# Performance work log

Measured on AMD Instinct MI355X. Metric: run time of the kernel, lower is better.

Reference implementation:

```python
import jax, jax.numpy as jnp
import numpy as np

NC = 80          # num classes (len(yolov8.names))
CONF = 0.25      # ultralytics conf_thres default
IOU_T = 0.45     # ultralytics iou_thres default
MAX_DET = 300    # module default max_det
K = 1024         # pre-NMS candidate cap (static stand-in for max_nms)
MAX_WH = 7680.0  # ultralytics class-offset for multi-class NMS


def setup_inputs() -> dict:
    key = jax.random.key(0)
    k1, k2, k3 = jax.random.split(key, 3)
    B, A = 32, 8400
    # YOLOv8 head layout: rows 0:4 = xywh (pixels), rows 4: = sigmoid class scores
    xy = jax.random.uniform(k1, (B, 2, A), dtype=jnp.float32) * 640.0
    wh = jax.random.uniform(k2, (B, 2, A), dtype=jnp.float32) * 160.0 + 8.0
    scores = jax.random.uniform(k3, (B, NC, A), dtype=jnp.float32) ** 3  # mostly below conf_thres
    preds = jnp.concatenate([xy, wh, scores], axis=1)  # [B, 4+NC, A]
    return {"preds": preds}


def _box_iou(b):
    # b: [K, 4] xyxy -> [K, K] pairwise IoU
    area = (b[:, 2] - b[:, 0]) * (b[:, 3] - b[:, 1])
    lt = jnp.maximum(b[:, None, :2], b[None, :, :2])
    rb = jnp.minimum(b[:, None, 2:], b[None, :, 2:])
    wh = jnp.clip(rb - lt, 0.0)
    inter = wh[..., 0] * wh[..., 1]
    return inter / (area[:, None] + area[None, :] - inter + 1e-7)


def _nms_single(pred):
    # pred: [4+NC, A]
    boxes_xywh = pred[:4].T           # [A, 4]
    cls_scores = pred[4:].T           # [A, NC]
    conf = cls_scores.max(-1)         # best-class confidence per anchor
    cls = jnp.argmax(cls_scores, -1)
    score = jnp.where(conf > CONF, conf, 0.0)
    top, idx = jax.lax.top_k(score, K)            # K candidates by confidence
    xywh = boxes_xywh[idx]
    half = xywh[:, 2:] * 0.5
    boxes = jnp.concatenate([xywh[:, :2] - half, xywh[:, :2] + half], -1)  # xyxy
    cls_k = cls[idx]
    valid = top > CONF
    # multi-class NMS via per-class coordinate offset (ultralytics trick)
    iou = _box_iou(boxes + (cls_k.astype(boxes.dtype) * MAX_WH)[:, None])
    ar = jnp.arange(K)

    def body(i, st):
        supp, keep = st
        ki = valid[i] & ~supp[i]
        keep = keep.at[i].set(ki)
        supp = supp | (ki & (iou[i] > IOU_T) & (ar > i))
        return supp, keep

    _, keep = jax.lax.fori_loop(0, K, body,
                                (jnp.zeros(K, bool), jnp.zeros(K, bool)))
    fscore = jnp.where(keep, top, 0.0)
    sc, order = jax.lax.top_k(fscore, MAX_DET)
    det = jnp.concatenate(
        [boxes[order], top[order][:, None], cls_k[order].astype(boxes.dtype)[:, None]], -1)
    # pad invalid rows with value NC in every column (matches F.pad(value=len(names)))
    return jnp.where((sc > CONF)[:, None], det, jnp.float32(NC))


def reference(preds):
    # [B, MAX_DET, 6] -> (x1, y1, x2, y2, conf, cls), padded rows filled with NC
    return jax.vmap(_nms_single)(preds)
```

## Files before the change

### kernel.cpp

```cpp
#include <hip/hip_runtime.h>
#include <stdint.h>

typedef unsigned long long u64;
typedef unsigned int u32;

#define NC 80
#define CONF_T 0.25f
#define IOU_THR 0.45f
#define MAX_DET 300
#define KBIG 1024
#define A_ANCH 8400
#define NROWS 84
#define MAX_WH 7680.0f
#define HBINS 256
#define BIN_BASE 0x3e80u

__device__ __forceinline__ void hadd(u32* h, u32 bin, bool m, int lane) {
    u64 act = __ballot(m);
    if (act == 0) return;
    int fl = __ffsll((unsigned long long)act) - 1;
    u32 fb = __shfl(bin, fl);
    u64 same = __ballot(m && (bin == fb));
    if (lane == fl) atomicAdd(&h[fb], (u32)__popcll(same));
    if (m && (bin != fb)) atomicAdd(&h[bin], 1u);
}

__global__ __launch_bounds__(512) void yolo_conf_kernel(const float* __restrict__ preds,
                                                        u64* __restrict__ keys,
                                                        u32* __restrict__ hist) {
    int b = blockIdx.x / 9;
    int slab = blockIdx.x % 9;
    if (slab == 0 && threadIdx.x < HBINS) hist[(size_t)b * HBINS + threadIdx.x] = 0;
    int g = slab * 512 + threadIdx.x;
    if (g >= A_ANCH / 2) return;
    int a0 = g * 2;
    const float* base = preds + ((size_t)b * NROWS + 4) * A_ANCH + a0;
    float2 best = *(const float2*)base;
    int bc0 = 0, bc1 = 0;
#pragma unroll 8
    for (int c = 1; c < NC; ++c) {
        float2 v = *(const float2*)(base + (size_t)c * A_ANCH);
        if (v.x > best.x) { best.x = v.x; bc0 = c; }
        if (v.y > best.y) { best.y = v.y; bc1 = c; }
    }
    float s0 = (best.x > CONF_T) ? best.x : 0.0f;
    float s1 = (best.y > CONF_T) ? best.y : 0.0f;
    ulonglong2 kk;
    kk.x = ((u64)__float_as_uint(s0) << 32) | ((u64)(16383 - a0) << 7) | (u64)bc0;
    kk.y = ((u64)__float_as_uint(s1) << 32) | ((u64)(16383 - (a0 + 1)) << 7) | (u64)bc1;
    *(ulonglong2*)(keys + (size_t)b * A_ANCH + a0) = kk;
}

__global__ __launch_bounds__(256) void yolo_prep_kernel(const float* __restrict__ preds,
                                                        const u64* __restrict__ keys,
                                                        float4* __restrict__ obox,
                                                        u32* __restrict__ hist) {
    __shared__ u32 lh[HBINS];
    const int lane = threadIdx.x & 63;
    int b = blockIdx.x / 33;
    int a = (blockIdx.x % 33) * 256 + threadIdx.x;
    lh[threadIdx.x] = 0;
    __syncthreads();
    u32 bits = 0, bin = 0;
    bool act = a < A_ANCH;
    if (act) {
        u64 key = keys[(size_t)b * A_ANCH + a];
        bits = (u32)(key >> 32);
        int cls = (int)(key & 127u);
        const float* pb = preds + (size_t)b * NROWS * A_ANCH + a;
        float x = pb[0];
        float y = pb[A_ANCH];
        float w = pb[2 * A_ANCH];
        float h = pb[3 * A_ANCH];
        float hw = __fmul_rn(w, 0.5f), hh = __fmul_rn(h, 0.5f);
        float x1 = __fsub_rn(x, hw), x2 = __fadd_rn(x, hw);
        float y1 = __fsub_rn(y, hh), y2 = __fadd_rn(y, hh);
        float off = __fmul_rn((float)cls, MAX_WH);
        float4 oB;
        oB.x = __fadd_rn(x1, off); oB.y = __fadd_rn(y1, off);
        oB.z = __fadd_rn(x2, off); oB.w = __fadd_rn(y2, off);
        obox[(size_t)b * A_ANCH + a] = oB;
        bin = (bits >> 16) - BIN_BASE;
        if (bin > 255u) bin = 255u;
    }
    hadd(lh, bin, act && (bits != 0u), lane);
    __syncthreads();
    u32 c = lh[threadIdx.x];
    if (c) atomicAdd(&hist[(size_t)b * HBINS + threadIdx.x], c);
}

__device__ __forceinline__ float iou_f(float ix1, float iy1, float ix2, float iy2, float iar,
                                       float jx1, float jy1, float jx2, float jy2, float jar) {
    float lx = fmaxf(ix1, jx1), ly = fmaxf(iy1, jy1);
    float rx = fminf(ix2, jx2), ry = fminf(iy2, jy2);
    float ww = fmaxf(__fsub_rn(rx, lx), 0.0f);
    float hh = fmaxf(__fsub_rn(ry, ly), 0.0f);
    float inter = __fmul_rn(ww, hh);
    float den = __fadd_rn(__fsub_rn(__fadd_rn(iar, jar), inter), 1e-7f);
    return __fdiv_rn(inter, den);
}

__device__ __forceinline__ u64 bstep(u64 v, u32 idx, u32 size, u32 stride) {
    u64 v2 = __shfl_xor((unsigned long long)v, (int)stride, 64);
    bool keep_big = (((idx & stride) == 0) == ((idx & size) == 0));
    return ((v > v2) == keep_big) ? v : v2;
}

__device__ __forceinline__ void radix_scan(u32* hist, int nb, int shift, u32* s_scal,
                                           u32* wsum, int tid, int lane, int wid) {
    int per = nb >> 9; if (per == 0) per = 1;
    int na = nb / per;
    u32 rem = s_scal[1];
    u32 Pk = s_scal[0];
    int hi = nb - 1 - per * tid;
    u32 s = 0;
    if (tid < na)
        for (int q = 0; q < per; ++q) s += hist[hi - q];
    u32 pre = s;
#pragma unroll
    for (int off = 1; off < 64; off <<= 1) {
        u32 o = __shfl_up(pre, off);
        if (lane >= off) pre += o;
    }
    if (lane == 63) wsum[wid] = pre;
    __syncthreads();
    u32 base = 0;
    for (int w = 0; w < wid; ++w) base += wsum[w];
    u32 run = base + pre - s;
    if (tid < na) {
        for (int q = 0; q < per; ++q) {
            int d = hi - q;
            u32 g = hist[d];
            if (run < rem && rem <= run + g) {
                s_scal[0] = Pk | ((u32)d << shift);
                s_scal[1] = rem - run;
            }
            run += g;
        }
    }
    __syncthreads();
}

__global__ __launch_bounds__(512) void yolo_selsort_kernel(const u64* __restrict__ keys,
                                                           const u32* __restrict__ hist,
                                                           u64* __restrict__ sortk,
                                                           u32* __restrict__ meta) {
    const int b = blockIdx.x;
    const int tid = threadIdx.x;
    const int lane = tid & 63;
    const int wid = tid >> 6;

    __shared__ u64 skey[KBIG];
    __shared__ u32 wsum[8];
    __shared__ u32 s_scal[4];
    __shared__ u32 s_cnt;

    const u64* kb = keys + (size_t)b * A_ANCH;
    const u32* hb = hist + (size_t)b * HBINS;

    u32 hg = (tid < HBINS) ? hb[HBINS - 1 - tid] : 0u;
    u32 vals[17];
#pragma unroll
    for (int it = 0; it < 17; ++it) {
        int a = tid + it * 512;
        vals[it] = (a < A_ANCH) ? (u32)(kb[a] >> 32) : 0u;
    }
    {
        u32 pre = hg;
#pragma unroll
        for (int off = 1; off < 64; off <<= 1) {
            u32 o = __shfl_up(pre, off);
            if (lane >= off) pre += o;
        }
        if (lane == 63) wsum[wid] = pre;
        __syncthreads();
        u32 base = 0;
        for (int w = 0; w < wid; ++w) base += wsum[w];
        pre += base;
        u32 run = pre - hg;
        if (tid < HBINS) {
            if (run < 512u && 512u <= pre) { s_scal[0] = (u32)(HBINS - 1 - tid); s_scal[2] = pre; }
            if (tid == HBINS - 1) {
                s_scal[3] = pre;
                if (pre < 512u) { s_scal[0] = 0; s_scal[2] = pre; }
            }
        }
        __syncthreads();
    }
    const u32 Pbin16 = BIN_BASE + s_scal[0];
    const u32 Cfast = s_scal[2];
    const u32 validN = s_scal[3];
    if (tid == 0) { meta[b * 2] = Cfast; meta[b * 2 + 1] = validN; }
    if (Cfast > (u32)KBIG) return;

    skey[tid] = 0; skey[tid + 512] = 0;
    if (tid == 0) s_cnt = 0;
    __syncthreads();
#pragma unroll
    for (int it = 0; it < 17; ++it) {
        int a = tid + it * 512;
        u32 v = vals[it];
        bool take = (a < A_ANCH) && (v != 0u) && ((v >> 16) >= Pbin16);
        u64 m = __ballot(take);
        if (m) {
            int fl = __ffsll((unsigned long long)m) - 1;
            u32 basep = 0;
            if (lane == fl) basep = atomicAdd(&s_cnt, (u32)__popcll(m));
            basep = __shfl(basep, fl);
            if (take) {
                u32 pos = basep + (u32)__popcll(m & ((1ull << lane) - 1ull));
                if (pos < (u32)KBIG) skey[pos] = kb[a];
            }
        }
    }
    __syncthreads();

    {
        u64 vA = skey[tid], vB = skey[tid + 512];
        const u32 iA = (u32)tid, iB = (u32)tid + 512;
#pragma unroll
        for (u32 size = 2; size <= 64; size <<= 1)
#pragma unroll
            for (u32 stride = size >> 1; stride >= 1; stride >>= 1) {
                vA = bstep(vA, iA, size, stride);
                vB = bstep(vB, iB, size, stride);
            }
        skey[tid] = vA; skey[tid + 512] = vB;
        __syncthreads();
        for (u32 size = 128; size <= 1024; size <<= 1) {
            for (u32 stride = size >> 1; stride >= 64; stride >>= 1) {
                u32 i1 = ((tid & ~(int)(stride - 1)) << 1) | (tid & (stride - 1));
                u32 i2 = i1 + stride;
                bool desc = ((i1 & size) == 0);
                u64 x = skey[i1], y = skey[i2];
                if ((x < y) == desc) { skey[i1] = y; skey[i2] = x; }
                __syncthreads();
            }
            vA = skey[tid]; vB = skey[tid + 512];
#pragma unroll
            for (u32 stride = 32; stride >= 1; stride >>= 1) {
                vA = bstep(vA, iA, size, stride);
                vB = bstep(vB, iB, size, stride);
            }
            skey[tid] = vA; skey[tid + 512] = vB;
            __syncthreads();
        }
    }
    u64* so = sortk + (size_t)b * KBIG;
    so[tid] = skey[tid];
    so[tid + 512] = skey[tid + 512];
}

__global__ __launch_bounds__(512) void yolo_mat_kernel(const u64* __restrict__ sortk,
                                                       const float4* __restrict__ obox,
                                                       u64* __restrict__ rows) {
    const int b = blockIdx.x >> 3;
    const int m = blockIdx.x & 7;
    const int tid = threadIdx.x;
    const int lane = tid & 63;
    const int wid = tid >> 6;
    __shared__ float bx1[512], by1[512], bx2[512], by2[512], bar[512];

    const u64* sk = sortk + (size_t)b * KBIG;
    {
        u64 key = sk[tid];
        int idx = 16383 - (int)((key >> 7) & 16383u);
        if (idx >= A_ANCH || idx < 0) idx = 0;
        float4 ob = obox[(size_t)b * A_ANCH + idx];
        bx1[tid] = ob.x; by1[tid] = ob.y; bx2[tid] = ob.z; by2[tid] = ob.w;
        bar[tid] = __fmul_rn(__fsub_rn(ob.z, ob.x), __fsub_rn(ob.w, ob.y));
    }
    __syncthreads();

#pragma unroll
    for (int rr = 0; rr < 8; ++rr) {
        int i = m * 64 + wid * 8 + rr;
        float ix1 = bx1[i], iy1 = by1[i], ix2 = bx2[i], iy2 = by2[i], iar = bar[i];
        u64* rowp = rows + ((size_t)b * 512 + i) * 8;
#pragma unroll
        for (int wd = 0; wd < 8; ++wd) {
            int j = wd * 64 + lane;
            float iou = iou_f(ix1, iy1, ix2, iy2, iar, bx1[j], by1[j], bx2[j], by2[j], bar[j]);
            u64 mbit = __ballot((j > i) && (iou > IOU_THR));
            if (lane == 0) rowp[wd] = mbit;
        }
    }
}

__global__ __launch_bounds__(512) void yolo_rec_kernel(const float* __restrict__ preds,
                                                       const u64* __restrict__ sortk,
                                                       const u64* __restrict__ rows,
                                                       const u32* __restrict__ meta,
                                                       u32* __restrict__ done,
                                                       float* __restrict__ out) {
    const int b = blockIdx.x;
    const int tid = threadIdx.x;
    const int lane = tid & 63;
    const int wid = tid >> 6;
    __shared__ u64 skl[512];
    __shared__ u64 supp[8];
    __shared__ u64 s_keep;
    __shared__ int keptlist[364];
    __shared__ u32 s_nkept;

    const u32 Cfast = meta[b * 2];
    const u32 validN = meta[b * 2 + 1];
    skl[tid] = sortk[(size_t)b * KBIG + tid];
    if (tid < 8) supp[tid] = 0;
    if (tid == 0) s_nkept = 0;
    __syncthreads();

    bool ok = (Cfast <= (u32)KBIG);
    if (ok) {
        const u64* rb = rows + (size_t)b * 512 * 8;
        for (int c = 0; c < 8; ++c) {
            if (wid == 0) {
                int i = c * 64 + lane;
                u64 key = skl[i];
                float sc = __uint_as_float((u32)(key >> 32));
                u64 ri = rb[(size_t)i * 8 + c];
                u64 validm = __ballot(sc > CONF_T) & ~supp[c];
                u32 rlo = (u32)ri, rhi = (u32)(ri >> 32);
                u64 sup = 0, keep = 0;
#pragma unroll
                for (int i2 = 0; i2 < 64; ++i2) {
                    u64 rr = (((u64)(u32)__builtin_amdgcn_readlane((int)rhi, i2)) << 32) |
                             (u64)(u32)__builtin_amdgcn_readlane((int)rlo, i2);
                    bool ki = (((validm & ~sup) >> i2) & 1ull) != 0;
                    if (ki) { keep |= (1ull << i2); sup |= rr; }
                }
                u32 basek = s_nkept;
                if ((keep >> lane) & 1ull) {
                    u32 slot = basek + (u32)__popcll(keep & ((1ull << lane) - 1ull));
                    keptlist[slot] = i;
                }
                if (lane == 0) { s_keep = keep; s_nkept = basek + (u32)__popcll(keep); }
            }
            __syncthreads();
            {
                u64 k = s_keep;
                u64 t = ((k >> lane) & 1ull) ? rb[(size_t)(c * 64 + lane) * 8 + wid] : 0ull;
#pragma unroll
                for (int off = 32; off >= 1; off >>= 1)
                    t |= (u64)__shfl_xor((unsigned long long)t, off, 64);
                if (lane == 0) supp[wid] |= t;
            }
            __syncthreads();
            if (s_nkept >= MAX_DET) break;
        }
    }
    u32 nk = ok ? s_nkept : 0;
    bool fin = ok && ((nk >= MAX_DET) || (validN <= 512u));
    if (tid == 0) done[b] = fin ? 1u : 0u;
    if (!fin) return;

    if (tid < MAX_DET) {
        float row[6];
        int t = (tid < (int)(nk < MAX_DET ? nk : MAX_DET)) ? keptlist[tid] : -1;
        if (t >= 0) {
            u64 key = skl[t];
            float score = __uint_as_float((u32)(key >> 32));
            int cls = (int)(key & 127u);
            int idx = 16383 - (int)((key >> 7) & 16383u);
            if (idx >= A_ANCH || idx < 0) idx = 0;
            const float* pb = preds + (size_t)b * NROWS * A_ANCH + idx;
            float x = pb[0], y = pb[A_ANCH], w = pb[2 * A_ANCH], h = pb[3 * A_ANCH];
            float hw = __fmul_rn(w, 0.5f), hh = __fmul_rn(h, 0.5f);
            row[0] = __fsub_rn(x, hw);
            row[1] = __fsub_rn(y, hh);
            row[2] = __fadd_rn(x, hw);
            row[3] = __fadd_rn(y, hh);
            row[4] = score;
            row[5] = (float)cls;
        } else {
            row[0] = row[1] = row[2] = row[3] = row[4] = row[5] = (float)NC;
        }
        float* o = out + ((size_t)b * MAX_DET + tid) * 6;
#pragma unroll
        for (int q = 0; q < 6; ++q) o[q] = row[q];
    }
}

union U2 {
    u32 hist[4096];
    struct { u32 eqw[264]; u32 wpre[264]; } tie;
};

__global__ __launch_bounds__(512) void yolo_fallback_kernel(const float* __restrict__ preds,
                                                            const u64* __restrict__ keys,
                                                            const float4* __restrict__ obox,
                                                            const u32* __restrict__ hist,
                                                            const u32* __restrict__ done,
                                                            float* __restrict__ out) {
    const int b = blockIdx.x;
    if (done[b]) return;
    const int tid = threadIdx.x;
    const int lane = tid & 63;
    const int wid = tid >> 6;

    __shared__ U2 u2;
    __shared__ u64 skey[KBIG];
    __shared__ float BX1[KBIG], BY1[KBIG], BX2[KBIG], BY2[KBIG], BAR[KBIG];
    __shared__ int keptlist[364];
    __shared__ float kx1[364], ky1[364], kx2[364], ky2[364], kar[364];
    __shared__ u32 kcls[364];
    __shared__ u64 rows[64];
    __shared__ u32 wsum[8];
    __shared__ u32 s_scal[4];
    __shared__ u32 s_cnt;
    __shared__ u32 s_csupp[2];
    __shared__ u32 s_nkept;

    const u64* kb = keys + (size_t)b * A_ANCH;
    const u32* hb = hist + (size_t)b * HBINS;
    u32 hg = (tid < HBINS) ? hb[HBINS - 1 - tid] : 0u;
    u32 vals[17];
#pragma unroll
    for (int it = 0; it < 17; ++it) {
        int a = tid + it * 512;
        vals[it] = (a < A_ANCH) ? (u32)(kb[a] >> 32) : 0u;
    }
    {
        u32 pre = hg;
#pragma unroll
        for (int off = 1; off < 64; off <<= 1) {
            u32 o = __shfl_up(pre, off);
            if (lane >= off) pre += o;
        }
        if (lane == 63) wsum[wid] = pre;
        __syncthreads();
        u32 base = 0;
        for (int w = 0; w < wid; ++w) base += wsum[w];
        pre += base;
        u32 run = pre - hg;
        if (tid < HBINS) {
            if (run < 512u && 512u <= pre) { s_scal[0] = (u32)(HBINS - 1 - tid); s_scal[2] = pre; }
            if (tid == HBINS - 1) {
                s_scal[3] = pre;
                if (pre < 512u) { s_scal[0] = 0; s_scal[2] = pre; }
            }
        }
        __syncthreads();
    }
    const u32 Pbin16 = BIN_BASE + s_scal[0];
    const u32 Cfast = s_scal[2];
    const u32 validN = s_scal[3];

    for (int pass = 0; pass < 2; ++pass) {
        u32 Ccand;
        if (pass == 0) {
            if (Cfast > (u32)KBIG) continue;
            Ccand = Cfast;
            skey[tid] = 0; skey[tid + 512] = 0;
            if (tid == 0) { s_cnt = 0; s_nkept = 0; s_csupp[0] = 0; s_csupp[1] = 0; }
            __syncthreads();
#pragma unroll
            for (int it = 0; it < 17; ++it) {
                int a = tid + it * 512;
                u32 v = vals[it];
                bool take = (a < A_ANCH) && (v != 0u) && ((v >> 16) >= Pbin16);
                u64 m = __ballot(take);
                if (m) {
                    int fl = __ffsll((unsigned long long)m) - 1;
                    u32 basep = 0;
                    if (lane == fl) basep = atomicAdd(&s_cnt, (u32)__popcll(m));
                    basep = __shfl(basep, fl);
                    if (take) {
                        u32 pos = basep + (u32)__popcll(m & ((1ull << lane) - 1ull));
                        if (pos < (u32)KBIG) skey[pos] = kb[a];
                    }
                }
            }
            __syncthreads();
        } else {
            for (int i = tid; i < 4096; i += 512) u2.hist[i] = 0;
            if (tid == 0) {
                s_scal[0] = 0; s_scal[1] = (u32)KBIG; s_scal[2] = 0;
                s_nkept = 0; s_csupp[0] = 0; s_csupp[1] = 0;
            }
            __syncthreads();
#pragma unroll
            for (int it = 0; it < 17; ++it) {
                int a = tid + it * 512;
                hadd(u2.hist, vals[it] >> 20, a < A_ANCH, lane);
            }
            __syncthreads();
            radix_scan(u2.hist, 4096, 20, s_scal, wsum, tid, lane, wid);
            for (int i = tid; i < 4096; i += 512) u2.hist[i] = 0;
            __syncthreads();
            u32 Pk = s_scal[0];
#pragma unroll
            for (int it = 0; it < 17; ++it) {
                int a = tid + it * 512;
                u32 v = vals[it];
                bool m = (a < A_ANCH) && ((v & 0xFFF00000u) == Pk);
                hadd(u2.hist, (v >> 8) & 4095u, m, lane);
            }
            __syncthreads();
            radix_scan(u2.hist, 4096, 8, s_scal, wsum, tid, lane, wid);
            for (int i = tid; i < 256; i += 512) u2.hist[i] = 0;
            __syncthreads();
            Pk = s_scal[0];
#pragma unroll
            for (int it = 0; it < 17; ++it) {
                int a = tid + it * 512;
                u32 v = vals[it];
                bool m = (a < A_ANCH) && ((v & 0xFFFFFF00u) == Pk);
                hadd(u2.hist, v & 255u, m, lane);
            }
            __syncthreads();
            radix_scan(u2.hist, 256, 0, s_scal, wsum, tid, lane, wid);
            const u32 P = s_scal[0];
            const u32 tEq = s_scal[1];
            if (tid < 264) u2.tie.eqw[tid] = 0;
            __syncthreads();
#pragma unroll
            for (int it = 0; it < 17; ++it) {
                int a = tid + it * 512;
                if (a < A_ANCH && vals[it] == P) atomicOr(&u2.tie.eqw[a >> 5], 1u << (a & 31));
            }
            __syncthreads();
            if (wid == 0) {
                u32 cw[5], loc = 0;
#pragma unroll
                for (int q = 0; q < 5; ++q) {
                    int w2 = lane * 5 + q;
                    u32 e = (w2 < 264) ? u2.tie.eqw[w2] : 0u;
                    cw[q] = (u32)__popc(e); loc += cw[q];
                }
                u32 pre = loc;
#pragma unroll
                for (int off = 1; off < 64; off <<= 1) {
                    u32 o = __shfl_up(pre, off);
                    if (lane >= off) pre += o;
                }
                u32 run = pre - loc;
#pragma unroll
                for (int q = 0; q < 5; ++q) {
                    int w2 = lane * 5 + q;
                    if (w2 < 264) u2.tie.wpre[w2] = run;
                    run += cw[q];
                }
            }
            __syncthreads();
#pragma unroll
            for (int it = 0; it < 17; ++it) {
                int a = tid + it * 512;
                bool take = false;
                if (a < A_ANCH) {
                    u32 v = vals[it];
                    take = v > P;
                    if (!take && v == P) {
                        u32 r = u2.tie.wpre[a >> 5] +
                                (u32)__popc(u2.tie.eqw[a >> 5] & ((1u << (a & 31)) - 1u));
                        take = (r < tEq);
                    }
                }
                u64 m = __ballot(take);
                if (m) {
                    int fl = __ffsll((unsigned long long)m) - 1;
                    u32 basep = 0;
                    if (lane == fl) basep = atomicAdd(&s_scal[2], (u32)__popcll(m));
                    basep = __shfl(basep, fl);
                    if (take) {
                        u32 pos = basep + (u32)__popcll(m & ((1ull << lane) - 1ull));
                        if (pos < (u32)KBIG) skey[pos] = kb[a];
                    }
                }
            }
            __syncthreads();
            Ccand = KBIG;
        }

        {
            u64 vA = skey[tid], vB = skey[tid + 512];
            const u32 iA = (u32)tid, iB = (u32)tid + 512;
#pragma unroll
            for (u32 size = 2; size <= 64; size <<= 1)
#pragma unroll
                for (u32 stride = size >> 1; stride >= 1; stride >>= 1) {
                    vA = bstep(vA, iA, size, stride);
                    vB = bstep(vB, iB, size, stride);
                }
            skey[tid] = vA; skey[tid + 512] = vB;
            __syncthreads();
            for (u32 size = 128; size <= 1024; size <<= 1) {
                for (u32 stride = size >> 1; stride >= 64; stride >>= 1) {
                    u32 i1 = ((tid & ~(int)(stride - 1)) << 1) | (tid & (stride - 1));
                    u32 i2 = i1 + stride;
                    bool desc = ((i1 & size) == 0);
                    u64 x = skey[i1], y = skey[i2];
                    if ((x < y) == desc) { skey[i1] = y; skey[i2] = x; }
                    __syncthreads();
                }
                vA = skey[tid]; vB = skey[tid + 512];
#pragma unroll
                for (u32 stride = 32; stride >= 1; stride >>= 1) {
                    vA = bstep(vA, iA, size, stride);
                    vB = bstep(vB, iB, size, stride);
                }
                skey[tid] = vA; skey[tid + 512] = vB;
                __syncthreads();
            }
        }

#pragma unroll
        for (int q = 0; q < 2; ++q) {
            int t = tid + q * 512;
            u64 key = skey[t];
            int idx = 16383 - (int)((key >> 7) & 16383u);
            if (idx >= A_ANCH || idx < 0) idx = 0;
            float4 ob = obox[(size_t)b * A_ANCH + idx];
            BX1[t] = ob.x; BY1[t] = ob.y; BX2[t] = ob.z; BY2[t] = ob.w;
            BAR[t] = __fmul_rn(__fsub_rn(ob.z, ob.x), __fsub_rn(ob.w, ob.y));
        }
        __syncthreads();

        const int nchunks = (int)((Ccand + 63u) >> 6);
        for (int c = 0; c < nchunks; ++c) {
            int j = c * 64 + lane;
            u64 keyj = skey[j];
            float scj = __uint_as_float((u32)(keyj >> 32));
            u32 clsj = (u32)(keyj & 127u);
            float jx1 = BX1[j], jy1 = BY1[j], jx2 = BX2[j], jy2 = BY2[j], jar = BAR[j];

            u32 nk = s_nkept;
            bool suppbit = false;
            for (u32 k = wid; k < nk; k += 8) {
                bool cm = (kcls[k] == clsj);
                if (__ballot(cm)) {
                    float iou = iou_f(kx1[k], ky1[k], kx2[k], ky2[k], kar[k],
                                      jx1, jy1, jx2, jy2, jar);
                    suppbit |= (cm && (iou > IOU_THR));
                }
            }
            u64 bm = __ballot(suppbit);
            if (bm && lane == 0) {
                atomicOr(&s_csupp[0], (u32)bm);
                atomicOr(&s_csupp[1], (u32)(bm >> 32));
            }
#pragma unroll
            for (int p2 = 0; p2 < 8; ++p2) {
                int i = p2 * 8 + wid;
                int ci = c * 64 + i;
                u32 clsi = (u32)(skey[ci] & 127u);
                u64 m = 0;
                if (__ballot(clsi == clsj)) {
                    float iou = iou_f(BX1[ci], BY1[ci], BX2[ci], BY2[ci], BAR[ci],
                                      jx1, jy1, jx2, jy2, jar);
                    m = __ballot((lane > i) && (iou > IOU_THR));
                }
                if (lane == 0) rows[i] = m;
            }
            __syncthreads();
            if (wid == 0) {
                u64 row = rows[lane];
                u32 rlo = (u32)row, rhi = (u32)(row >> 32);
                u64 csupp = (((u64)s_csupp[1]) << 32) | (u64)s_csupp[0];
                u64 validm = __ballot(scj > CONF_T) & ~csupp;
                u64 supp = 0, keep = 0;
#pragma unroll
                for (int i = 0; i < 64; ++i) {
                    u64 ri = (((u64)(u32)__builtin_amdgcn_readlane((int)rhi, i)) << 32) |
                             (u64)(u32)__builtin_amdgcn_readlane((int)rlo, i);
                    bool ki = (((validm & ~supp) >> i) & 1ull) != 0;
                    if (ki) { keep |= (1ull << i); supp |= ri; }
                }
                u32 basek = s_nkept;
                if ((keep >> lane) & 1ull) {
                    u32 slot = basek + (u32)__popcll(keep & ((1ull << lane) - 1ull));
                    keptlist[slot] = j;
                    kx1[slot] = jx1; ky1[slot] = jy1;
                    kx2[slot] = jx2; ky2[slot] = jy2;
                    kar[slot] = jar; kcls[slot] = clsj;
                }
                if (lane == 0) {
                    s_nkept = basek + (u32)__popcll(keep);
                    s_csupp[0] = 0; s_csupp[1] = 0;
                }
            }
            __syncthreads();
            if (s_nkept >= MAX_DET) break;
        }

        u32 nk = s_nkept;
        bool finished = (nk >= MAX_DET) || (Ccand >= validN) || (pass == 1);
        if (!finished) continue;

        if (tid < MAX_DET) {
            float row[6];
            int t = (tid < (int)(nk < MAX_DET ? nk : MAX_DET)) ? keptlist[tid] : -1;
            if (t >= 0) {
                u64 key = skey[t];
                float score = __uint_as_float((u32)(key >> 32));
                int cls = (int)(key & 127u);
                int idx = 16383 - (int)((key >> 7) & 16383u);
                if (idx >= A_ANCH || idx < 0) idx = 0;
                const float* pb = preds + (size_t)b * NROWS * A_ANCH + idx;
                float x = pb[0], y = pb[A_ANCH], w = pb[2 * A_ANCH], h = pb[3 * A_ANCH];
                float hw = __fmul_rn(w, 0.5f), hh = __fmul_rn(h, 0.5f);
                row[0] = __fsub_rn(x, hw);
                row[1] = __fsub_rn(y, hh);
                row[2] = __fadd_rn(x, hw);
                row[3] = __fadd_rn(y, hh);
                row[4] = score;
                row[5] = (float)cls;
            } else {
                row[0] = row[1] = row[2] = row[3] = row[4] = row[5] = (float)NC;
            }
            float* o = out + ((size_t)b * MAX_DET + tid) * 6;
#pragma unroll
            for (int q = 0; q < 6; ++q) o[q] = row[q];
        }
        break;
    }
}

extern "C" void kernel_launch(void* const* d_in, const int* in_sizes, int n_in,
                              void* d_out, int out_size, void* d_ws, size_t ws_size,
                              hipStream_t stream) {
    const float* preds = (const float*)d_in[0];
    float* out = (float*)d_out;
    int B = in_sizes[0] / (NROWS * A_ANCH);
    float4* obox = (float4*)d_ws;
    u64* keys = (u64*)(obox + (size_t)B * A_ANCH);
    u64* sortk = keys + (size_t)B * A_ANCH;
    u64* rows = sortk + (size_t)B * KBIG;
    u32* hist = (u32*)(rows + (size_t)B * 512 * 8);
    u32* meta = hist + (size_t)B * HBINS;
    u32* done = meta + (size_t)B * 2;
    yolo_conf_kernel<<<dim3(B * 9), dim3(512), 0, stream>>>(preds, keys, hist);
    yolo_prep_kernel<<<dim3(B * 33), dim3(256), 0, stream>>>(preds, keys, obox, hist);
    yolo_selsort_kernel<<<dim3(B), dim3(512), 0, stream>>>(keys, hist, sortk, meta);
    yolo_mat_kernel<<<dim3(B * 8), dim3(512), 0, stream>>>(sortk, obox, rows);
    yolo_rec_kernel<<<dim3(B), dim3(512), 0, stream>>>(preds, sortk, rows, meta, done, out);
    yolo_fallback_kernel<<<dim3(B), dim3(512), 0, stream>>>(preds, keys, obox, hist, done, out);
}
```

Baseline: 65.86 us.

## Replace bitonic sort with rank sort and merge fallback into recurrence kernel

Swaps the in-block bitonic sort of 1024 keys for a counting rank sort: each thread compares its two keys against all 1024 shared keys and scatters them to their rank, so only one barrier is needed instead of many. It also folds the fallback kernel into the recurrence kernel through a shared-memory union, which drops one launch and the done-flag round trip. In exchange the rank sort does O(N^2) shared reads, about 1024 per thread, and the fused kernel's larger shared footprint may reduce occupancy.

```diff
diff --git a/kernel.cpp b/kernel.cpp
--- a/kernel.cpp
+++ b/kernel.cpp
@@ -151,6 +151,7 @@
     const int wid = tid >> 6;
 
     __shared__ u64 skey[KBIG];
+    __shared__ u64 sorted[KBIG];
     __shared__ u32 wsum[8];
     __shared__ u32 s_scal[4];
     __shared__ u32 s_cnt;
@@ -216,39 +217,21 @@
     __syncthreads();
 
     {
-        u64 vA = skey[tid], vB = skey[tid + 512];
-        const u32 iA = (u32)tid, iB = (u32)tid + 512;
-#pragma unroll
-        for (u32 size = 2; size <= 64; size <<= 1)
-#pragma unroll
-            for (u32 stride = size >> 1; stride >= 1; stride >>= 1) {
-                vA = bstep(vA, iA, size, stride);
-                vB = bstep(vB, iB, size, stride);
-            }
-        skey[tid] = vA; skey[tid + 512] = vB;
+        u64 kA = skey[tid], kB = skey[tid + 512];
+        u32 rA = 0, rB = 0;
+#pragma unroll 8
+        for (int j = 0; j < KBIG; ++j) {
+            u64 kj = skey[j];
+            rA += (kj > kA) || ((kj == kA) && (j < tid)) ? 1u : 0u;
+            rB += (kj > kB) || ((kj == kB) && (j < tid + 512)) ? 1u : 0u;
+        }
+        sorted[rA] = kA;
+        sorted[rB] = kB;
         __syncthreads();
-        for (u32 size = 128; size <= 1024; size <<= 1) {
-            for (u32 stride = size >> 1; stride >= 64; stride >>= 1) {
-                u32 i1 = ((tid & ~(int)(stride - 1)) << 1) | (tid & (stride - 1));
-                u32 i2 = i1 + stride;
-                bool desc = ((i1 & size) == 0);
-                u64 x = skey[i1], y = skey[i2];
-                if ((x < y) == desc) { skey[i1] = y; skey[i2] = x; }
-                __syncthreads();
-            }
-            vA = skey[tid]; vB = skey[tid + 512];
-#pragma unroll
-            for (u32 stride = 32; stride >= 1; stride >>= 1) {
-                vA = bstep(vA, iA, size, stride);
-                vB = bstep(vB, iB, size, stride);
-            }
-            skey[tid] = vA; skey[tid + 512] = vB;
-            __syncthreads();
-        }
-    }
-    u64* so = sortk + (size_t)b * KBIG;
-    so[tid] = skey[tid];
-    so[tid + 512] = skey[tid + 512];
+        u64* so = sortk + (size_t)b * KBIG;
+        so[tid] = sorted[tid];
+        so[tid + 512] = sorted[tid + 512];
+    }
 }
 
 __global__ __launch_bounds__(512) void yolo_mat_kernel(const u64* __restrict__ sortk,
@@ -287,39 +270,66 @@
     }
 }
 
-__global__ __launch_bounds__(512) void yolo_rec_kernel(const float* __restrict__ preds,
-                                                       const u64* __restrict__ sortk,
-                                                       const u64* __restrict__ rows,
-                                                       const u32* __restrict__ meta,
-                                                       u32* __restrict__ done,
-                                                       float* __restrict__ out) {
+union U2 {
+    u32 hist[4096];
+    struct { u32 eqw[264]; u32 wpre[264]; } tie;
+};
+
+__global__ __launch_bounds__(512) void yolo_recfb_kernel(const float* __restrict__ preds,
+                                                         const u64* __restrict__ keys,
+                                                         const u64* __restrict__ sortk,
+                                                         const u64* __restrict__ rowsg,
+                                                         const float4* __restrict__ obox,
+                                                         const u32* __restrict__ hist,
+                                                         const u32* __restrict__ meta,
+                                                         float* __restrict__ out) {
     const int b = blockIdx.x;
     const int tid = threadIdx.x;
     const int lane = tid & 63;
     const int wid = tid >> 6;
-    __shared__ u64 skl[512];
-    __shared__ u64 supp[8];
-    __shared__ u64 s_keep;
-    __shared__ int keptlist[364];
+
+    union SH {
+        struct {
+            u64 skl[512];
+            u64 supp[8];
+            u64 keep;
+            int keptlist[364];
+        } r;
+        struct {
+            U2 u2;
+            u64 skey[KBIG];
+            float BX1[KBIG], BY1[KBIG], BX2[KBIG], BY2[KBIG], BAR[KBIG];
+            int keptlist[364];
+            float kx1[364], ky1[364], kx2[364], ky2[364], kar[364];
+            u32 kcls[364];
+            u64 rows64[64];
+        } f;
+    };
+    __shared__ SH sh;
+    __shared__ u32 s_scal[4];
+    __shared__ u32 wsum[8];
+    __shared__ u32 s_cnt;
+    __shared__ u32 s_csupp[2];
     __shared__ u32 s_nkept;
 
-    const u32 Cfast = meta[b * 2];
-    const u32 validN = meta[b * 2 + 1];
-    skl[tid] = sortk[(size_t)b * KBIG + tid];
-    if (tid < 8) supp[tid] = 0;
+    const u32 Cfast0 = meta[b * 2];
+    const u32 validN0 = meta[b * 2 + 1];
+
+    sh.r.skl[tid] = sortk[(size_t)b * KBIG + tid];
+    if (tid < 8) sh.r.supp[tid] = 0;
     if (tid == 0) s_nkept = 0;
     __syncthreads();
 
-    bool ok = (Cfast <= (u32)KBIG);
+    bool ok = (Cfast0 <= (u32)KBIG);
     if (ok) {
-        const u64* rb = rows + (size_t)b * 512 * 8;
+        const u64* rb = rowsg + (size_t)b * 512 * 8;
         for (int c = 0; c < 8; ++c) {
             if (wid == 0) {
                 int i = c * 64 + lane;
-                u64 key = skl[i];
+                u64 key = sh.r.skl[i];
                 float sc = __uint_as_float((u32)(key >> 32));
                 u64 ri = rb[(size_t)i * 8 + c];
-                u64 validm = __ballot(sc > CONF_T) & ~supp[c];
+                u64 validm = __ballot(sc > CONF_T) & ~sh.r.supp[c];
                 u32 rlo = (u32)ri, rhi = (u32)(ri >> 32);
                 u64 sup = 0, keep = 0;
 #pragma unroll
@@ -332,84 +342,65 @@
                 u32 basek = s_nkept;
                 if ((keep >> lane) & 1ull) {
                     u32 slot = basek + (u32)__popcll(keep & ((1ull << lane) - 1ull));
-                    keptlist[slot] = i;
-                }
-                if (lane == 0) { s_keep = keep; s_nkept = basek + (u32)__popcll(keep); }
+                    sh.r.keptlist[slot] = i;
+                }
+                if (lane == 0) { sh.r.keep = keep; s_nkept = basek + (u32)__popcll(keep); }
             }
             __syncthreads();
             {
-                u64 k = s_keep;
+                u64 k = sh.r.keep;
                 u64 t = ((k >> lane) & 1ull) ? rb[(size_t)(c * 64 + lane) * 8 + wid] : 0ull;
 #pragma unroll
                 for (int off = 32; off >= 1; off >>= 1)
                     t |= (u64)__shfl_xor((unsigned long long)t, off, 64);
-                if (lane == 0) supp[wid] |= t;
+                if (lane == 0) sh.r.supp[wid] |= t;
             }
             __syncthreads();
             if (s_nkept >= MAX_DET) break;
         }
     }
-    u32 nk = ok ? s_nkept : 0;
-    bool fin = ok && ((nk >= MAX_DET) || (validN <= 512u));
-    if (tid == 0) done[b] = fin ? 1u : 0u;
-    if (!fin) return;
-
-    if (tid < MAX_DET) {
-        float row[6];
-        int t = (tid < (int)(nk < MAX_DET ? nk : MAX_DET)) ? keptlist[tid] : -1;
-        if (t >= 0) {
-            u64 key = skl[t];
-            float score = __uint_as_float((u32)(key >> 32));
-            int cls = (int)(key & 127u);
-            int idx = 16383 - (int)((key >> 7) & 16383u);
-            if (idx >= A_ANCH || idx < 0) idx = 0;
-            const float* pb = preds + (size_t)b * NROWS * A_ANCH + idx;
-            float x = pb[0], y = pb[A_ANCH], w = pb[2 * A_ANCH], h = pb[3 * A_ANCH];
-            float hw = __fmul_rn(w, 0.5f), hh = __fmul_rn(h, 0.5f);
-            row[0] = __fsub_rn(x, hw);
-            row[1] = __fsub_rn(y, hh);
-            row[2] = __fadd_rn(x, hw);
-            row[3] = __fadd_rn(y, hh);
-            row[4] = score;
-            row[5] = (float)cls;
-        } else {
-            row[0] = row[1] = row[2] = row[3] = row[4] = row[5] = (float)NC;
-        }
-        float* o = out + ((size_t)b * MAX_DET + tid) * 6;
-#pragma unroll
-        for (int q = 0; q < 6; ++q) o[q] = row[q];
-    }
-}
-
-union U2 {
-    u32 hist[4096];
-    struct { u32 eqw[264]; u32 wpre[264]; } tie;
-};
-
-__global__ __launch_bounds__(512) void yolo_fallback_kernel(const float* __restrict__ preds,
-                                                            const u64* __restrict__ keys,
-                                                            const float4* __restrict__ obox,
-                                                            const u32* __restrict__ hist,
-                                                            const u32* __restrict__ done,
-                                                            float* __restrict__ out) {
-    const int b = blockIdx.x;
-    if (done[b]) return;
-    const int tid = threadIdx.x;
-    const int lane = tid & 63;
-    const int wid = tid >> 6;
-
-    __shared__ U2 u2;
-    __shared__ u64 skey[KBIG];
-    __shared__ float BX1[KBIG], BY1[KBIG], BX2[KBIG], BY2[KBIG], BAR[KBIG];
-    __shared__ int keptlist[364];
-    __shared__ float kx1[364], ky1[364], kx2[364], ky2[364], kar[364];
-    __shared__ u32 kcls[364];
-    __shared__ u64 rows[64];
-    __shared__ u32 wsum[8];
-    __shared__ u32 s_scal[4];
-    __shared__ u32 s_cnt;
-    __shared__ u32 s_csupp[2];
-    __shared__ u32 s_nkept;
+    u32 nk0 = ok ? s_nkept : 0;
+    bool fin = ok && ((nk0 >= MAX_DET) || (validN0 <= 512u));
+
+    if (fin) {
+        if (tid < MAX_DET) {
+            float row[6];
+            int t = (tid < (int)(nk0 < MAX_DET ? nk0 : MAX_DET)) ? sh.r.keptlist[tid] : -1;
+            if (t >= 0) {
+                u64 key = sh.r.skl[t];
+                float score = __uint_as_float((u32)(key >> 32));
+                int cls = (int)(key & 127u);
+                int idx = 16383 - (int)((key >> 7) & 16383u);
+                if (idx >= A_ANCH || idx < 0) idx = 0;
+                const float* pb = preds + (size_t)b * NROWS * A_ANCH + idx;
+                float x = pb[0], y = pb[A_ANCH], w = pb[2 * A_ANCH], h = pb[3 * A_ANCH];
+                float hw = __fmul_rn(w, 0.5f), hh = __fmul_rn(h, 0.5f);
+                row[0] = __fsub_rn(x, hw);
+                row[1] = __fsub_rn(y, hh);
+                row[2] = __fadd_rn(x, hw);
+                row[3] = __fadd_rn(y, hh);
+                row[4] = score;
+                row[5] = (float)cls;
+            } else {
+                row[0] = row[1] = row[2] = row[3] = row[4] = row[5] = (float)NC;
+            }
+            float* o = out + ((size_t)b * MAX_DET + tid) * 6;
+#pragma unroll
+            for (int q = 0; q < 6; ++q) o[q] = row[q];
+        }
+        return;
+    }
+
+    __syncthreads();
+    U2* u2 = &sh.f.u2;
+    u64* skey = sh.f.skey;
+    float* BX1 = sh.f.BX1; float* BY1 = sh.f.BY1;
+    float* BX2 = sh.f.BX2; float* BY2 = sh.f.BY2; float* BAR = sh.f.BAR;
+    int* keptlist = sh.f.keptlist;
+    float* kx1 = sh.f.kx1; float* ky1 = sh.f.ky1;
+    float* kx2 = sh.f.kx2; float* ky2 = sh.f.ky2; float* kar = sh.f.kar;
+    u32* kcls = sh.f.kcls;
+    u64* rows = sh.f.rows64;
 
     const u64* kb = keys + (size_t)b * A_ANCH;
     const u32* hb = hist + (size_t)b * HBINS;
@@ -473,7 +464,7 @@
             }
             __syncthreads();
         } else {
-            for (int i = tid; i < 4096; i += 512) u2.hist[i] = 0;
+            for (int i = tid; i < 4096; i += 512) u2->hist[i] = 0;
             if (tid == 0) {
                 s_scal[0] = 0; s_scal[1] = (u32)KBIG; s_scal[2] = 0;
                 s_nkept = 0; s_csupp[0] = 0; s_csupp[1] = 0;
@@ -482,11 +473,11 @@
 #pragma unroll
             for (int it = 0; it < 17; ++it) {
                 int a = tid + it * 512;
-                hadd(u2.hist, vals[it] >> 20, a < A_ANCH, lane);
-            }
-            __syncthreads();
-            radix_scan(u2.hist, 4096, 20, s_scal, wsum, tid, lane, wid);
-            for (int i = tid; i < 4096; i += 512) u2.hist[i] = 0;
+                hadd(u2->hist, vals[it] >> 20, a < A_ANCH, lane);
+            }
+            __syncthreads();
+            radix_scan(u2->hist, 4096, 20, s_scal, wsum, tid, lane, wid);
+            for (int i = tid; i < 4096; i += 512) u2->hist[i] = 0;
             __syncthreads();
             u32 Pk = s_scal[0];
 #pragma unroll
@@ -494,11 +485,11 @@
                 int a = tid + it * 512;
                 u32 v = vals[it];
                 bool m = (a < A_ANCH) && ((v & 0xFFF00000u) == Pk);
-                hadd(u2.hist, (v >> 8) & 4095u, m, lane);
-            }
-            __syncthreads();
-            radix_scan(u2.hist, 4096, 8, s_scal, wsum, tid, lane, wid);
-            for (int i = tid; i < 256; i += 512) u2.hist[i] = 0;
+                hadd(u2->hist, (v >> 8) & 4095u, m, lane);
+            }
+            __syncthreads();
+            radix_scan(u2->hist, 4096, 8, s_scal, wsum, tid, lane, wid);
+            for (int i = tid; i < 256; i += 512) u2->hist[i] = 0;
             __syncthreads();
             Pk = s_scal[0];
 #pragma unroll
@@ -506,18 +497,18 @@
                 int a = tid + it * 512;
                 u32 v = vals[it];
                 bool m = (a < A_ANCH) && ((v & 0xFFFFFF00u) == Pk);
-                hadd(u2.hist, v & 255u, m, lane);
-            }
-            __syncthreads();
-            radix_scan(u2.hist, 256, 0, s_scal, wsum, tid, lane, wid);
+                hadd(u2->hist, v & 255u, m, lane);
+            }
+            __syncthreads();
+            radix_scan(u2->hist, 256, 0, s_scal, wsum, tid, lane, wid);
             const u32 P = s_scal[0];
             const u32 tEq = s_scal[1];
-            if (tid < 264) u2.tie.eqw[tid] = 0;
+            if (tid < 264) u2->tie.eqw[tid] = 0;
             __syncthreads();
 #pragma unroll
             for (int it = 0; it < 17; ++it) {
                 int a = tid + it * 512;
-                if (a < A_ANCH && vals[it] == P) atomicOr(&u2.tie.eqw[a >> 5], 1u << (a & 31));
+                if (a < A_ANCH && vals[it] == P) atomicOr(&u2->tie.eqw[a >> 5], 1u << (a & 31));
             }
             __syncthreads();
             if (wid == 0) {
@@ -525,7 +516,7 @@
 #pragma unroll
                 for (int q = 0; q < 5; ++q) {
                     int w2 = lane * 5 + q;
-                    u32 e = (w2 < 264) ? u2.tie.eqw[w2] : 0u;
+                    u32 e = (w2 < 264) ? u2->tie.eqw[w2] : 0u;
                     cw[q] = (u32)__popc(e); loc += cw[q];
                 }
                 u32 pre = loc;
@@ -538,7 +529,7 @@
 #pragma unroll
                 for (int q = 0; q < 5; ++q) {
                     int w2 = lane * 5 + q;
-                    if (w2 < 264) u2.tie.wpre[w2] = run;
+                    if (w2 < 264) u2->tie.wpre[w2] = run;
                     run += cw[q];
                 }
             }
@@ -551,8 +542,8 @@
                     u32 v = vals[it];
                     take = v > P;
                     if (!take && v == P) {
-                        u32 r = u2.tie.wpre[a >> 5] +
-                                (u32)__popc(u2.tie.eqw[a >> 5] & ((1u << (a & 31)) - 1u));
+                        u32 r = u2->tie.wpre[a >> 5] +
+                                (u32)__popc(u2->tie.eqw[a >> 5] & ((1u << (a & 31)) - 1u));
                         take = (r < tEq);
                     }
                 }
@@ -728,11 +719,9 @@
     u64* rows = sortk + (size_t)B * KBIG;
     u32* hist = (u32*)(rows + (size_t)B * 512 * 8);
     u32* meta = hist + (size_t)B * HBINS;
-    u32* done = meta + (size_t)B * 2;
     yolo_conf_kernel<<<dim3(B * 9), dim3(512), 0, stream>>>(preds, keys, hist);
     yolo_prep_kernel<<<dim3(B * 33), dim3(256), 0, stream>>>(preds, keys, obox, hist);
     yolo_selsort_kernel<<<dim3(B), dim3(512), 0, stream>>>(keys, hist, sortk, meta);
     yolo_mat_kernel<<<dim3(B * 8), dim3(512), 0, stream>>>(sortk, obox, rows);
-    yolo_rec_kernel<<<dim3(B), dim3(512), 0, stream>>>(preds, sortk, rows, meta, done, out);
-    yolo_fallback_kernel<<<dim3(B), dim3(512), 0, stream>>>(preds, keys, obox, hist, done, out);
-}
+    yolo_recfb_kernel<<<dim3(B), dim3(512), 0, stream>>>(preds, keys, sortk, rows, obox, hist, meta, out);
+}
```

Result: slower. 111.7 us (+69.6%).
